# Performance work log

Measured on AMD Instinct MI355X. Metric: run time of the kernel, lower is better.

Reference implementation:

```python
import jax, jax.numpy as jnp
import numpy as np

BETA = 0.95      # config.snn_beta
THR = 1.0        # snntorch Leaky default threshold
SLOPE = 10.0     # config.surrogate_slope (fast_sigmoid)
T = 16           # config.snn_timesteps
A_PLUS, A_MINUS = 0.008, 0.01
ELIG_DECAY = 0.95

# Heaviside spike with fast-sigmoid surrogate gradient: d/dm = 1/(slope*|m-thr|+1)^2
@jax.custom_vjp
def spike_fn(m):
    return (m > THR).astype(m.dtype)

def _spk_fwd(m):
    return spike_fn(m), m

def _spk_bwd(m, g):
    return (g / (SLOPE * jnp.abs(m - THR) + 1.0) ** 2,)

spike_fn.defvjp(_spk_fwd, _spk_bwd)


def setup_inputs() -> dict:
    key = jax.random.key(0)
    ks = jax.random.split(key, 7)
    B, S, H, A = 65536, 25, 64, 4

    def lin_w(k, o, i):
        lim = 1.0 / np.sqrt(i)
        return jax.random.uniform(k, (o, i), jnp.float32, -lim, lim)

    def lin_b(k, o, i):
        lim = 1.0 / np.sqrt(i)
        return jax.random.uniform(k, (o,), jnp.float32, -lim, lim)

    return {
        "x": jax.random.normal(ks[0], (B, S), jnp.float32),
        "W1": lin_w(ks[1], H, S), "b1": lin_b(ks[2], H, S),
        "W2": lin_w(ks[3], H, H), "b2": lin_b(ks[4], H, H),
        "W3": lin_w(ks[5], A, H), "b3": lin_b(ks[6], A, H),
        "elig0": jnp.zeros((A, H), jnp.float32),  # eligibility trace (fc3.out, fc3.in)
    }


def reference(x, W1, b1, W2, b2, W3, b3, elig0):
    B = x.shape[0]
    H = W1.shape[0]
    A = W3.shape[0]
    cur1 = x @ W1.T + b1  # input current is identical every timestep

    def step(carry, _):
        m1, m2, m3, elig, acc = carry
        m1 = BETA * m1 + cur1
        s1 = spike_fn(m1)
        m1 = m1 - s1 * THR
        m2 = BETA * m2 + s1 @ W2.T + b2
        s2 = spike_fn(m2)
        m2 = m2 - s2 * THR
        m3 = BETA * m3 + s2 @ W3.T + b3
        s3 = spike_fn(m3)
        m3 = m3 - s3 * THR
        pre = jax.lax.stop_gradient(s2).mean(0)   # [H]
        post = jax.lax.stop_gradient(s3).mean(0)  # [A]
        elig = ELIG_DECAY * elig + (A_PLUS - A_MINUS) * jnp.outer(post, pre)
        return (m1, m2, m3, elig, acc + s3), None

    init = (
        jnp.zeros((B, H), x.dtype),
        jnp.zeros((B, H), x.dtype),
        jnp.zeros((B, A), x.dtype),
        elig0,
        jnp.zeros((B, A), x.dtype),
    )
    (_, _, _, elig, acc), _ = jax.lax.scan(step, init, None, length=T)
    readout = acc / T  # mean over timesteps of spk3
    probs = jax.nn.softmax(readout, axis=-1)
    return probs, elig
```

## Files before the change

### kernel.cpp

```cpp
#include <hip/hip_runtime.h>

#define T_STEPS 16
#define H 64
#define S_IN 25
#define A_OUT 4
#define NB 65536
#define UPW 8
#define WPB 8
#define EPB 128

typedef unsigned long long ull;

__device__ __forceinline__ float fmaf_(float a, float b, float c) { return __builtin_fmaf(a, b, c); }

__global__ void snn_prep(const float* __restrict__ W2, const float* __restrict__ W3,
                         float* __restrict__ W2T, float* __restrict__ W3T) {
    int i = blockIdx.x * blockDim.x + threadIdx.x;
    if (i < H * H) { int h = i >> 6, k = i & 63; W2T[k * H + h] = W2[h * H + k]; }
    if (i < A_OUT * H) { int a = i >> 6, h = i & 63; W3T[h * A_OUT + a] = W3[a * H + h]; }
}

__global__ __launch_bounds__(512, 4) __attribute__((amdgpu_waves_per_eu(4, 4)))
void snn_main(
    const float* __restrict__ x,
    const float* __restrict__ W1, const float* __restrict__ b1,
    const float* __restrict__ W2T, const float* __restrict__ b2,
    const float* __restrict__ W3T, const float* __restrict__ b3,
    float* __restrict__ out, int* __restrict__ g_pre, int* __restrict__ g_post)
{
#pragma clang fp contract(off)
    __shared__ float s1f[H][EPB];
    __shared__ float4 w3s[H];
    __shared__ unsigned int s2buf[2][WPB][EPB];
    __shared__ float m3acc[EPB][8];
    __shared__ int lds_pre[T_STEPS * H];
    __shared__ int lds_post[T_STEPS * A_OUT];

    const int tid = threadIdx.x;
    if (tid < H) w3s[tid] = reinterpret_cast<const float4*>(W3T)[tid];
    for (int i = tid; i < T_STEPS * H; i += 512) lds_pre[i] = 0;
    if (tid < T_STEPS * A_OUT) lds_post[tid] = 0;
    for (int i = tid; i < EPB * 8; i += 512) (&m3acc[0][0])[i] = 0.0f;

    const int lane  = tid & 63;
    const int wq    = __builtin_amdgcn_readfirstlane(tid >> 6);
    const int hbase = UPW * wq;
    const int bA    = blockIdx.x * EPB + lane;
    const int bB    = bA + 64;

    float cur1A[UPW], cur1B[UPW];
    {
        float xv[S_IN];
        #pragma unroll
        for (int s = 0; s < S_IN; ++s) xv[s] = x[bA * S_IN + s];
        #pragma unroll
        for (int j = 0; j < UPW; ++j) {
            int h = hbase + j;
            float acc = 0.0f;
            #pragma unroll
            for (int s = 0; s < S_IN; ++s) acc = fmaf_(xv[s], W1[h * S_IN + s], acc);
            cur1A[j] = acc + b1[h];
        }
        #pragma unroll
        for (int s = 0; s < S_IN; ++s) xv[s] = x[bB * S_IN + s];
        #pragma unroll
        for (int j = 0; j < UPW; ++j) {
            int h = hbase + j;
            float acc = 0.0f;
            #pragma unroll
            for (int s = 0; s < S_IN; ++s) acc = fmaf_(xv[s], W1[h * S_IN + s], acc);
            cur1B[j] = acc + b1[h];
        }
    }

    float m1A[UPW], m1B[UPW], m2A[UPW], m2B[UPW];
    #pragma unroll
    for (int j = 0; j < UPW; ++j) { m1A[j] = 0.0f; m1B[j] = 0.0f; m2A[j] = 0.0f; m2B[j] = 0.0f; }

    __syncthreads();

    #pragma unroll
    for (int j = 0; j < UPW; ++j) {
        float ma = 0.95f * m1A[j]; ma = ma + cur1A[j];
        bool pa = ma > 1.0f; m1A[j] = pa ? (ma - 1.0f) : ma;
        s1f[hbase + j][lane] = pa ? 1.0f : 0.0f;
        float mb = 0.95f * m1B[j]; mb = mb + cur1B[j];
        bool pb = mb > 1.0f; m1B[j] = pb ? (mb - 1.0f) : mb;
        s1f[hbase + j][lane + 64] = pb ? 1.0f : 0.0f;
    }
    __syncthreads();

    for (int t = 0; t < T_STEPS; ++t) {
        const int slot = t & 1;

        #pragma unroll
        for (int j = 0; j < UPW; ++j) { m2A[j] = 0.95f * m2A[j]; m2B[j] = 0.95f * m2B[j]; }

        #pragma unroll 8
        for (int k = 0; k < H; ++k) {
            const float sfA = s1f[k][lane];
            const float sfB = s1f[k][lane + 64];
            const float* wr = W2T + k * H + hbase;
            #pragma unroll
            for (int j = 0; j < UPW; ++j) {
                const float w = wr[j];
                m2A[j] = fmaf_(sfA, w, m2A[j]);
                m2B[j] = fmaf_(sfB, w, m2B[j]);
            }
        }

        unsigned int s2A = 0u, s2B = 0u;
        int myCnt = 0;
        #pragma unroll
        for (int j = 0; j < UPW; ++j) {
            float ma = m2A[j] + b2[hbase + j];
            bool pa = ma > 1.0f;
            m2A[j] = ma - (pa ? 1.0f : 0.0f);
            s2A |= (pa ? 1u : 0u) << j;
            float mb = m2B[j] + b2[hbase + j];
            bool pb = mb > 1.0f;
            m2B[j] = mb - (pb ? 1.0f : 0.0f);
            s2B |= (pb ? 1u : 0u) << j;
            int cnt = (int)__popcll(__ballot(pa)) + (int)__popcll(__ballot(pb));
            myCnt = (lane == j) ? cnt : myCnt;
        }
        s2buf[slot][wq][lane] = s2A;
        s2buf[slot][wq][lane + 64] = s2B;
        if (lane < UPW) lds_pre[t * H + hbase + lane] = myCnt;

        __syncthreads();

        if (t < T_STEPS - 1) {
            #pragma unroll
            for (int j = 0; j < UPW; ++j) {
                float ma = 0.95f * m1A[j]; ma = ma + cur1A[j];
                bool pa = ma > 1.0f; m1A[j] = pa ? (ma - 1.0f) : ma;
                s1f[hbase + j][lane] = pa ? 1.0f : 0.0f;
                float mb = 0.95f * m1B[j]; mb = mb + cur1B[j];
                bool pb = mb > 1.0f; m1B[j] = pb ? (mb - 1.0f) : mb;
                s1f[hbase + j][lane + 64] = pb ? 1.0f : 0.0f;
            }
        }
        __syncthreads();

        const int duty = wq & 3;
        if (duty == (t & 3)) {
            const int el = (wq < 4) ? lane : (lane + 64);
            unsigned int q0 = s2buf[slot][0][el], q1 = s2buf[slot][1][el];
            unsigned int q2 = s2buf[slot][2][el], q3 = s2buf[slot][3][el];
            unsigned int q4 = s2buf[slot][4][el], q5 = s2buf[slot][5][el];
            unsigned int q6 = s2buf[slot][6][el], q7 = s2buf[slot][7][el];
            ull s2v = (ull)(q0 | (q1 << 8) | (q2 << 16) | (q3 << 24))
                    | ((ull)(q4 | (q5 << 8) | (q6 << 16) | (q7 << 24)) << 32);
            float m3[A_OUT], ac[A_OUT];
            #pragma unroll
            for (int a = 0; a < A_OUT; ++a) { m3[a] = 0.95f * m3acc[el][a]; ac[a] = m3acc[el][4 + a]; }
            for (int h = 0; h < H; ++h) {
                float s2f = (float)((unsigned)s2v & 1u);
                s2v >>= 1;
                const float4 w = w3s[h];
                m3[0] = fmaf_(s2f, w.x, m3[0]);
                m3[1] = fmaf_(s2f, w.y, m3[1]);
                m3[2] = fmaf_(s2f, w.z, m3[2]);
                m3[3] = fmaf_(s2f, w.w, m3[3]);
            }
            int myPost = 0;
            #pragma unroll
            for (int a = 0; a < A_OUT; ++a) {
                float m = m3[a] + b3[a];
                bool sp = m > 1.0f;
                float s3f = sp ? 1.0f : 0.0f;
                m3[a] = m - s3f;
                ac[a] = ac[a] + s3f;
                int c = (int)__popcll(__ballot(sp));
                myPost = (lane == a) ? c : myPost;
            }
            if (lane < A_OUT) atomicAdd(&lds_post[t * A_OUT + lane], myPost);
            if (t == T_STEPS - 1) {
                float r0 = ac[0] * 0.0625f, r1 = ac[1] * 0.0625f;
                float r2 = ac[2] * 0.0625f, r3 = ac[3] * 0.0625f;
                float mx = fmaxf(fmaxf(r0, r1), fmaxf(r2, r3));
                float e0 = expf(r0 - mx), e1 = expf(r1 - mx);
                float e2 = expf(r2 - mx), e3 = expf(r3 - mx);
                float s = ((e0 + e1) + e2) + e3;
                reinterpret_cast<float4*>(out)[blockIdx.x * EPB + el] =
                    make_float4(e0 / s, e1 / s, e2 / s, e3 / s);
            } else {
                #pragma unroll
                for (int a = 0; a < A_OUT; ++a) { m3acc[el][a] = m3[a]; m3acc[el][4 + a] = ac[a]; }
            }
        }
    }

    __syncthreads();
    for (int i = tid; i < T_STEPS * H; i += 512) atomicAdd(&g_pre[i], lds_pre[i]);
    if (tid < T_STEPS * A_OUT) atomicAdd(&g_post[tid], lds_post[tid]);
}

__global__ void snn_elig(const int* __restrict__ g_pre, const int* __restrict__ g_post,
                         const float* __restrict__ elig0, float* __restrict__ out) {
#pragma clang fp contract(off)
    int i = threadIdx.x;
    int a = i >> 6, h = i & 63;
    float e = elig0[i];
    const float invB = 1.0f / 65536.0f;
    for (int t = 0; t < T_STEPS; ++t) {
        float pre  = (float)g_pre[t * H + h] * invB;
        float post = (float)g_post[t * A_OUT + a] * invB;
        e = 0.95f * e + (-0.002f) * (post * pre);
    }
    out[NB * A_OUT + i] = e;
}

extern "C" void kernel_launch(void* const* d_in, const int* in_sizes, int n_in,
                              void* d_out, int out_size, void* d_ws, size_t ws_size,
                              hipStream_t stream) {
    const float* x     = (const float*)d_in[0];
    const float* W1    = (const float*)d_in[1];
    const float* b1    = (const float*)d_in[2];
    const float* W2    = (const float*)d_in[3];
    const float* b2    = (const float*)d_in[4];
    const float* W3    = (const float*)d_in[5];
    const float* b3    = (const float*)d_in[6];
    const float* elig0 = (const float*)d_in[7];
    float* out = (float*)d_out;

    char* ws = (char*)d_ws;
    int*   g_pre  = (int*)(ws);
    int*   g_post = (int*)(ws + 4096);
    float* W2T    = (float*)(ws + 8192);
    float* W3T    = (float*)(ws + 8192 + 16384);

    (void)hipMemsetAsync(ws, 0, 4096 + 256, stream);
    snn_prep<<<17, 256, 0, stream>>>(W2, W3, W2T, W3T);
    snn_main<<<NB / EPB, 512, 0, stream>>>(x, W1, b1, W2T, b2, W3T, b3, out, g_pre, g_post);
    snn_elig<<<1, 256, 0, stream>>>(g_pre, g_post, elig0, out);
}
```

Before: 156.0 us.

## Process four batch elements per lane and precompute layer-1 spikes as bitmasks

Each block now handles 256 elements, with four per lane instead of two. Every W2 weight load is therefore reused across four FMAs, and W2 is regrouped per wave so each wave reads a contiguous slice. Layer-1 membrane dynamics no longer depend on other layers, so all 16 timesteps of layer-1 spikes are computed up front and kept as 128-bit bitmasks, which removes per-step m1 state. The cost is more registers per thread (launch bounds drop to 2 blocks per EU), half as many blocks, and a reworked duty split for layer-3 work.

```diff
diff --git a/kernel.cpp b/kernel.cpp
--- a/kernel.cpp
+++ b/kernel.cpp
@@ -7,24 +7,26 @@
 #define NB 65536
 #define UPW 8
 #define WPB 8
-#define EPB 128
+#define EPB 256
 
 typedef unsigned long long ull;
 
 __device__ __forceinline__ float fmaf_(float a, float b, float c) { return __builtin_fmaf(a, b, c); }
 
 __global__ void snn_prep(const float* __restrict__ W2, const float* __restrict__ W3,
-                         float* __restrict__ W2T, float* __restrict__ W3T) {
+                         float* __restrict__ W2G, float* __restrict__ W3T) {
     int i = blockIdx.x * blockDim.x + threadIdx.x;
-    if (i < H * H) { int h = i >> 6, k = i & 63; W2T[k * H + h] = W2[h * H + k]; }
+    if (i < H * H) {
+        int wq = i >> 9, k = (i >> 3) & 63, j = i & 7;
+        W2G[i] = W2[(wq * 8 + j) * 64 + k];
+    }
     if (i < A_OUT * H) { int a = i >> 6, h = i & 63; W3T[h * A_OUT + a] = W3[a * H + h]; }
 }
 
-__global__ __launch_bounds__(512, 4) __attribute__((amdgpu_waves_per_eu(4, 4)))
-void snn_main(
+__global__ __launch_bounds__(512, 2) void snn_main(
     const float* __restrict__ x,
     const float* __restrict__ W1, const float* __restrict__ b1,
-    const float* __restrict__ W2T, const float* __restrict__ b2,
+    const float* __restrict__ W2G, const float* __restrict__ b2,
     const float* __restrict__ W3T, const float* __restrict__ b3,
     float* __restrict__ out, int* __restrict__ g_pre, int* __restrict__ g_post)
 {
@@ -45,107 +47,135 @@
     const int lane  = tid & 63;
     const int wq    = __builtin_amdgcn_readfirstlane(tid >> 6);
     const int hbase = UPW * wq;
-    const int bA    = blockIdx.x * EPB + lane;
-    const int bB    = bA + 64;
-
-    float cur1A[UPW], cur1B[UPW];
+    const int b0    = blockIdx.x * EPB + lane;
+
+    ull msk0[4], msk1[4];
     {
-        float xv[S_IN];
-        #pragma unroll
-        for (int s = 0; s < S_IN; ++s) xv[s] = x[bA * S_IN + s];
-        #pragma unroll
-        for (int j = 0; j < UPW; ++j) {
-            int h = hbase + j;
-            float acc = 0.0f;
-            #pragma unroll
-            for (int s = 0; s < S_IN; ++s) acc = fmaf_(xv[s], W1[h * S_IN + s], acc);
-            cur1A[j] = acc + b1[h];
-        }
-        #pragma unroll
-        for (int s = 0; s < S_IN; ++s) xv[s] = x[bB * S_IN + s];
-        #pragma unroll
-        for (int j = 0; j < UPW; ++j) {
-            int h = hbase + j;
-            float acc = 0.0f;
-            #pragma unroll
-            for (int s = 0; s < S_IN; ++s) acc = fmaf_(xv[s], W1[h * S_IN + s], acc);
-            cur1B[j] = acc + b1[h];
-        }
-    }
-
-    float m1A[UPW], m1B[UPW], m2A[UPW], m2B[UPW];
+        float cur1[4][UPW], m1[4][UPW];
+        #pragma unroll
+        for (int e = 0; e < 4; ++e) {
+            float xv[S_IN];
+            #pragma unroll
+            for (int s = 0; s < S_IN; ++s) xv[s] = x[(b0 + 64 * e) * S_IN + s];
+            #pragma unroll
+            for (int j = 0; j < UPW; ++j) {
+                int h = hbase + j;
+                float acc = 0.0f;
+                #pragma unroll
+                for (int s = 0; s < S_IN; ++s) acc = fmaf_(xv[s], W1[h * S_IN + s], acc);
+                cur1[e][j] = acc + b1[h];
+                m1[e][j] = 0.0f;
+            }
+            msk0[e] = 0ull; msk1[e] = 0ull;
+        }
+        for (int t = 0; t < 8; ++t) {
+            #pragma unroll
+            for (int e = 0; e < 4; ++e) {
+                unsigned int sm = 0u;
+                #pragma unroll
+                for (int j = 0; j < UPW; ++j) {
+                    float m = 0.95f * m1[e][j]; m = m + cur1[e][j];
+                    bool sp = m > 1.0f; m1[e][j] = sp ? (m - 1.0f) : m;
+                    sm |= (sp ? 1u : 0u) << j;
+                }
+                msk0[e] |= ((ull)sm) << (8 * t);
+            }
+        }
+        for (int t = 0; t < 8; ++t) {
+            #pragma unroll
+            for (int e = 0; e < 4; ++e) {
+                unsigned int sm = 0u;
+                #pragma unroll
+                for (int j = 0; j < UPW; ++j) {
+                    float m = 0.95f * m1[e][j]; m = m + cur1[e][j];
+                    bool sp = m > 1.0f; m1[e][j] = sp ? (m - 1.0f) : m;
+                    sm |= (sp ? 1u : 0u) << j;
+                }
+                msk1[e] |= ((ull)sm) << (8 * t);
+            }
+        }
+    }
+
     #pragma unroll
-    for (int j = 0; j < UPW; ++j) { m1A[j] = 0.0f; m1B[j] = 0.0f; m2A[j] = 0.0f; m2B[j] = 0.0f; }
-
-    __syncthreads();
-
+    for (int e = 0; e < 4; ++e) {
+        unsigned int u = (unsigned int)msk0[e] & 0xFFu;
+        #pragma unroll
+        for (int j = 0; j < UPW; ++j)
+            s1f[hbase + j][lane + 64 * e] = ((u >> j) & 1u) ? 1.0f : 0.0f;
+        msk0[e] = (msk0[e] >> 8) | (msk1[e] << 56); msk1[e] >>= 8;
+    }
+
+    float m2[4][UPW];
     #pragma unroll
-    for (int j = 0; j < UPW; ++j) {
-        float ma = 0.95f * m1A[j]; ma = ma + cur1A[j];
-        bool pa = ma > 1.0f; m1A[j] = pa ? (ma - 1.0f) : ma;
-        s1f[hbase + j][lane] = pa ? 1.0f : 0.0f;
-        float mb = 0.95f * m1B[j]; mb = mb + cur1B[j];
-        bool pb = mb > 1.0f; m1B[j] = pb ? (mb - 1.0f) : mb;
-        s1f[hbase + j][lane + 64] = pb ? 1.0f : 0.0f;
-    }
+    for (int e = 0; e < 4; ++e)
+    #pragma unroll
+    for (int j = 0; j < UPW; ++j) m2[e][j] = 0.0f;
+
+    const float* wbase = W2G + wq * 512;
+
     __syncthreads();
 
     for (int t = 0; t < T_STEPS; ++t) {
         const int slot = t & 1;
 
         #pragma unroll
-        for (int j = 0; j < UPW; ++j) { m2A[j] = 0.95f * m2A[j]; m2B[j] = 0.95f * m2B[j]; }
+        for (int e = 0; e < 4; ++e)
+        #pragma unroll
+        for (int j = 0; j < UPW; ++j) m2[e][j] = 0.95f * m2[e][j];
 
         #pragma unroll 8
         for (int k = 0; k < H; ++k) {
-            const float sfA = s1f[k][lane];
-            const float sfB = s1f[k][lane + 64];
-            const float* wr = W2T + k * H + hbase;
+            const float sf0 = s1f[k][lane];
+            const float sf1 = s1f[k][lane + 64];
+            const float sf2 = s1f[k][lane + 128];
+            const float sf3 = s1f[k][lane + 192];
+            const float* wr = wbase + k * 8;
             #pragma unroll
             for (int j = 0; j < UPW; ++j) {
                 const float w = wr[j];
-                m2A[j] = fmaf_(sfA, w, m2A[j]);
-                m2B[j] = fmaf_(sfB, w, m2B[j]);
-            }
-        }
-
-        unsigned int s2A = 0u, s2B = 0u;
+                m2[0][j] = fmaf_(sf0, w, m2[0][j]);
+                m2[1][j] = fmaf_(sf1, w, m2[1][j]);
+                m2[2][j] = fmaf_(sf2, w, m2[2][j]);
+                m2[3][j] = fmaf_(sf3, w, m2[3][j]);
+            }
+        }
+
         int myCnt = 0;
+        unsigned int s2m[4] = {0u, 0u, 0u, 0u};
         #pragma unroll
         for (int j = 0; j < UPW; ++j) {
-            float ma = m2A[j] + b2[hbase + j];
-            bool pa = ma > 1.0f;
-            m2A[j] = ma - (pa ? 1.0f : 0.0f);
-            s2A |= (pa ? 1u : 0u) << j;
-            float mb = m2B[j] + b2[hbase + j];
-            bool pb = mb > 1.0f;
-            m2B[j] = mb - (pb ? 1.0f : 0.0f);
-            s2B |= (pb ? 1u : 0u) << j;
-            int cnt = (int)__popcll(__ballot(pa)) + (int)__popcll(__ballot(pb));
+            int cnt = 0;
+            #pragma unroll
+            for (int e = 0; e < 4; ++e) {
+                float m = m2[e][j] + b2[hbase + j];
+                bool sp = m > 1.0f;
+                m2[e][j] = m - (sp ? 1.0f : 0.0f);
+                s2m[e] |= (sp ? 1u : 0u) << j;
+                cnt += (int)__popcll(__ballot(sp));
+            }
             myCnt = (lane == j) ? cnt : myCnt;
         }
-        s2buf[slot][wq][lane] = s2A;
-        s2buf[slot][wq][lane + 64] = s2B;
+        #pragma unroll
+        for (int e = 0; e < 4; ++e) s2buf[slot][wq][lane + 64 * e] = s2m[e];
         if (lane < UPW) lds_pre[t * H + hbase + lane] = myCnt;
 
         __syncthreads();
 
         if (t < T_STEPS - 1) {
             #pragma unroll
-            for (int j = 0; j < UPW; ++j) {
-                float ma = 0.95f * m1A[j]; ma = ma + cur1A[j];
-                bool pa = ma > 1.0f; m1A[j] = pa ? (ma - 1.0f) : ma;
-                s1f[hbase + j][lane] = pa ? 1.0f : 0.0f;
-                float mb = 0.95f * m1B[j]; mb = mb + cur1B[j];
-                bool pb = mb > 1.0f; m1B[j] = pb ? (mb - 1.0f) : mb;
-                s1f[hbase + j][lane + 64] = pb ? 1.0f : 0.0f;
-            }
-        }
+            for (int e = 0; e < 4; ++e) {
+                unsigned int u = (unsigned int)msk0[e] & 0xFFu;
+                #pragma unroll
+                for (int j = 0; j < UPW; ++j)
+                    s1f[hbase + j][lane + 64 * e] = ((u >> j) & 1u) ? 1.0f : 0.0f;
+                msk0[e] = (msk0[e] >> 8) | (msk1[e] << 56); msk1[e] >>= 8;
+            }
+        }
+
         __syncthreads();
 
-        const int duty = wq & 3;
-        if (duty == (t & 3)) {
-            const int el = (wq < 4) ? lane : (lane + 64);
+        if ((wq >> 2) == (t & 1)) {
+            const int el = (wq & 3) * 64 + lane;
             unsigned int q0 = s2buf[slot][0][el], q1 = s2buf[slot][1][el];
             unsigned int q2 = s2buf[slot][2][el], q3 = s2buf[slot][3][el];
             unsigned int q4 = s2buf[slot][4][el], q5 = s2buf[slot][5][el];
@@ -228,11 +258,11 @@
     char* ws = (char*)d_ws;
     int*   g_pre  = (int*)(ws);
     int*   g_post = (int*)(ws + 4096);
-    float* W2T    = (float*)(ws + 8192);
+    float* W2G    = (float*)(ws + 8192);
     float* W3T    = (float*)(ws + 8192 + 16384);
 
     (void)hipMemsetAsync(ws, 0, 4096 + 256, stream);
-    snn_prep<<<17, 256, 0, stream>>>(W2, W3, W2T, W3T);
-    snn_main<<<NB / EPB, 512, 0, stream>>>(x, W1, b1, W2T, b2, W3T, b3, out, g_pre, g_post);
+    snn_prep<<<17, 256, 0, stream>>>(W2, W3, W2G, W3T);
+    snn_main<<<NB / EPB, 512, 0, stream>>>(x, W1, b1, W2G, b2, W3T, b3, out, g_pre, g_post);
     snn_elig<<<1, 256, 0, stream>>>(g_pre, g_post, elig0, out);
 }
```

Result: slower. 178.2 us (+14.2%).
